# Kernel optimization log

Measured on AMD Instinct MI355X. Metric: run time of the kernel, lower is better.

## Reference

```python
import jax, jax.numpy as jnp
import numpy as np

EPS_S = 1e-06
EPS_R = 1e-06

def _gaussian_masks(mu, logsx, logsy, rho, H, W, dtype):
    # coordinate grid in [-1,1], grid[h,w] = (x, y)
    ys = jnp.linspace(-1.0, 1.0, H, dtype=dtype)
    xs = jnp.linspace(-1.0, 1.0, W, dtype=dtype)
    Y, X = jnp.meshgrid(ys, xs, indexing='ij')  # [H,W]
    sx = jnp.exp(logsx)[:, None, None] + EPS_S   # [n,1,1]
    sy = jnp.exp(logsy)[:, None, None] + EPS_S
    r = jnp.tanh(rho)[:, None, None]
    xc = (X[None] - mu[:, 0, None, None]) / sx   # [n,H,W]
    yc = (Y[None] - mu[:, 1, None, None]) / sy
    A = xc ** 2 + yc ** 2 - 2.0 * r * xc * yc
    denom = 2.0 * (1.0 - r ** 2 + EPS_R)
    return jnp.exp(-A / denom)                   # [n,H,W]

def setup_inputs() -> dict:
    key = jax.random.key(0)
    ks = jax.random.split(key, 6)
    B, C, H, W, n = 32, 256, 36, 64, 4096
    feat = jax.random.normal(ks[0], (B, C, H, W), dtype=jnp.float32)
    mu = jax.random.uniform(ks[1], (n, 2), dtype=jnp.float32) * 2.0 - 1.0
    logsx = jnp.zeros((n,), dtype=jnp.float32)
    logsy = jnp.zeros((n,), dtype=jnp.float32)
    rho = jnp.zeros((n,), dtype=jnp.float32)
    weight = jax.random.normal(ks[5], (n, C), dtype=jnp.float32) * 0.01
    return {"feat": feat, "mu": mu, "logsx": logsx, "logsy": logsy, "rho": rho, "weight": weight}

def reference(feat, mu, logsx, logsy, rho, weight):
    B, C, H, W = feat.shape
    G = _gaussian_masks(mu, logsx, logsy, rho, H, W, feat.dtype)  # [n,H,W]
    # pooled[b,n,c] = sum_{h,w} feat[b,c,h,w] * G[n,h,w]  (batched GEMM)
    pooled = jnp.einsum('bchw,nhw->bnc', feat, G)
    out = jnp.einsum('bnc,nc->bn', pooled, weight.astype(feat.dtype))
    return out
```

## Files before the change

kernel.cpp:

```cpp
#include <hip/hip_runtime.h>
#include <hip/hip_bf16.h>

#define P_HW   2304
#define NG     4096
#define NCOL   8192
#define KDIM   P_HW

typedef __bf16 bf16x8 __attribute__((ext_vector_type(8)));
typedef float  f32x4  __attribute__((ext_vector_type(4)));

__device__ __forceinline__ unsigned short f2bf(float f) {
    union { float f; unsigned int u; } x; x.f = f;
    unsigned int r = x.u + 0x7FFFu + ((x.u >> 16) & 1u);
    return (unsigned short)(r >> 16);
}

__global__ void mask_kernel(const float* __restrict__ mu,
                            const float* __restrict__ logsx,
                            const float* __restrict__ logsy,
                            const float* __restrict__ rho,
                            unsigned short* __restrict__ G) {
    const int n = blockIdx.x;
    const float mux = mu[2 * n], muy = mu[2 * n + 1];
    const float sx = __expf(logsx[n]) + 1e-6f;
    const float sy = __expf(logsy[n]) + 1e-6f;
    const float r  = tanhf(rho[n]);
    const float inv_den = 1.0f / (2.0f * (1.0f - r * r + 1e-6f));
    const float isx = 1.0f / sx, isy = 1.0f / sy;
    for (int base = threadIdx.x * 8; base < P_HW; base += 2048) {
        const int h = base >> 6, w0 = base & 63;
        const float Y  = -1.0f + (float)h * (2.0f / 35.0f);
        const float yc = (Y - muy) * isy;
        union { unsigned short s[8]; uint4 q; } o;
#pragma unroll
        for (int j = 0; j < 8; ++j) {
            const float X  = -1.0f + (float)(w0 + j) * (2.0f / 63.0f);
            const float xc = (X - mux) * isx;
            const float A  = xc * xc + yc * yc - 2.0f * r * xc * yc;
            o.s[j] = f2bf(__expf(-A * inv_den));
        }
        *(uint4*)&G[(size_t)n * P_HW + base] = o.q;
    }
}

__global__ void cast_feat(const float* __restrict__ feat,
                          unsigned short* __restrict__ F) {
    const size_t i = ((size_t)blockIdx.x * 256 + threadIdx.x) * 8;
    const float4 v0 = *(const float4*)(feat + i);
    const float4 v1 = *(const float4*)(feat + i + 4);
    union { unsigned short s[8]; uint4 q; } o;
    o.s[0] = f2bf(v0.x); o.s[1] = f2bf(v0.y); o.s[2] = f2bf(v0.z); o.s[3] = f2bf(v0.w);
    o.s[4] = f2bf(v1.x); o.s[5] = f2bf(v1.y); o.s[6] = f2bf(v1.z); o.s[7] = f2bf(v1.w);
    *(uint4*)(F + i) = o.q;
}

__device__ __forceinline__ void async16(const void* g, void* l) {
    __builtin_amdgcn_global_load_lds(
        (__attribute__((address_space(1))) void*)(unsigned long long)g,
        (__attribute__((address_space(3))) void*)(unsigned int)(unsigned long long)l,
        16, 0, 0);
}

__global__ __launch_bounds__(256) void gemm_fused(
    const unsigned short* __restrict__ G,
    const unsigned short* __restrict__ F,
    const float* __restrict__ weight,
    float* __restrict__ out)
{
    __shared__ __align__(16) unsigned short ldsA[128 * 64];
    __shared__ __align__(16) unsigned short ldsB[128 * 64];

    const int tid  = threadIdx.x;
    const int lane = tid & 63;
    const int wave = tid >> 6;
    const int waveM = wave >> 1, waveN = wave & 1;
    const int quad = lane >> 4, m = lane & 15;

    const int rowBase = blockIdx.y * 128;
    const int colBase = blockIdx.x * 128;

    const unsigned short* Aptr[4];
    const unsigned short* Bptr[4];
    int ldsOff[4];
#pragma unroll
    for (int i = 0; i < 4; ++i) {
        const int s  = i * 256 + tid;
        const int r  = s >> 3;
        const int cp = s & 7;
        const int c  = cp ^ (r & 7);
        Aptr[i] = G + (size_t)(rowBase + r) * KDIM + c * 8;
        Bptr[i] = F + (size_t)(colBase + r) * KDIM + c * 8;
        ldsOff[i] = s * 8;
    }

    f32x4 acc[4][4];
#pragma unroll
    for (int i = 0; i < 4; ++i)
#pragma unroll
        for (int j = 0; j < 4; ++j)
            acc[i][j] = (f32x4){0.f, 0.f, 0.f, 0.f};

    for (int k0 = 0; k0 < KDIM; k0 += 64) {
#pragma unroll
        for (int i = 0; i < 4; ++i) async16(Aptr[i] + k0, &ldsA[ldsOff[i]]);
#pragma unroll
        for (int i = 0; i < 4; ++i) async16(Bptr[i] + k0, &ldsB[ldsOff[i]]);
        __syncthreads();

#pragma unroll
        for (int h = 0; h < 2; ++h) {
            bf16x8 a[4], b[4];
#pragma unroll
            for (int i = 0; i < 4; ++i) {
                const int r  = waveM * 64 + i * 16 + m;
                const int cp = (h * 4 + quad) ^ (r & 7);
                a[i] = *(const bf16x8*)&ldsA[r * 64 + cp * 8];
            }
#pragma unroll
            for (int j = 0; j < 4; ++j) {
                const int r  = waveN * 64 + j * 16 + m;
                const int cp = (h * 4 + quad) ^ (r & 7);
                b[j] = *(const bf16x8*)&ldsB[r * 64 + cp * 8];
            }
#pragma unroll
            for (int i = 0; i < 4; ++i)
#pragma unroll
                for (int j = 0; j < 4; ++j)
                    acc[i][j] = __builtin_amdgcn_mfma_f32_16x16x32_bf16(a[i], b[j], acc[i][j], 0, 0, 0);
        }
        __syncthreads();
    }

    const int bidx  = colBase >> 8;
    const int cwave = (colBase & 255) + waveN * 64;
#pragma unroll
    for (int i = 0; i < 4; ++i) {
        const int nrow = rowBase + waveM * 64 + i * 16 + quad * 4;
#pragma unroll
        for (int reg = 0; reg < 4; ++reg) {
            const float* wrow = weight + (size_t)(nrow + reg) * 256 + cwave + m;
            float s = acc[i][0][reg] * wrow[0]
                    + acc[i][1][reg] * wrow[16]
                    + acc[i][2][reg] * wrow[32]
                    + acc[i][3][reg] * wrow[48];
            s += __shfl_xor(s, 1);
            s += __shfl_xor(s, 2);
            s += __shfl_xor(s, 4);
            s += __shfl_xor(s, 8);
            if (m == 0)
                atomicAdd(out + (size_t)bidx * NG + nrow + reg, s);
        }
    }
}

extern "C" void kernel_launch(void* const* d_in, const int* in_sizes, int n_in,
                              void* d_out, int out_size, void* d_ws, size_t ws_size,
                              hipStream_t stream) {
    const float* feat   = (const float*)d_in[0];
    const float* mu     = (const float*)d_in[1];
    const float* logsx  = (const float*)d_in[2];
    const float* logsy  = (const float*)d_in[3];
    const float* rho    = (const float*)d_in[4];
    const float* weight = (const float*)d_in[5];
    float* out = (float*)d_out;

    unsigned short* Gbuf = (unsigned short*)d_ws;
    unsigned short* Fbuf = Gbuf + (size_t)NG * P_HW;

    hipMemsetAsync(out, 0, (size_t)32 * NG * sizeof(float), stream);

    hipLaunchKernelGGL(mask_kernel, dim3(NG), dim3(256), 0, stream,
                       mu, logsx, logsy, rho, Gbuf);

    hipLaunchKernelGGL(cast_feat, dim3(9216), dim3(256), 0, stream, feat, Fbuf);

    hipLaunchKernelGGL(gemm_fused, dim3(NCOL / 128, NG / 128), dim3(256), 0, stream,
                       Gbuf, Fbuf, weight, out);
}
```

Before: 312.8 us.

## Switch GEMM to 32x32x16 MFMA and merge prep kernels into one launch

The GEMM inner loop now uses 32x32x16 bf16 MFMA with 2x2 tiles per wave instead of 16x16x32 with 4x4 tiles. This halves the MFMA instruction count per wave and changes the LDS fragment read pattern. The epilogue is reworked for the 32x32 accumulator layout and adds one more shuffle stage. The feature cast, mask generation and output zeroing are merged into one prep kernel, removing the memset and one launch.

```diff
diff --git a/kernel.cpp b/kernel.cpp
--- a/kernel.cpp
+++ b/kernel.cpp
@@ -7,7 +7,7 @@
 #define KDIM   P_HW
 
 typedef __bf16 bf16x8 __attribute__((ext_vector_type(8)));
-typedef float  f32x4  __attribute__((ext_vector_type(4)));
+typedef float  f32x16 __attribute__((ext_vector_type(16)));
 
 __device__ __forceinline__ unsigned short f2bf(float f) {
     union { float f; unsigned int u; } x; x.f = f;
@@ -15,43 +15,53 @@
     return (unsigned short)(r >> 16);
 }
 
-__global__ void mask_kernel(const float* __restrict__ mu,
-                            const float* __restrict__ logsx,
-                            const float* __restrict__ logsy,
-                            const float* __restrict__ rho,
-                            unsigned short* __restrict__ G) {
-    const int n = blockIdx.x;
-    const float mux = mu[2 * n], muy = mu[2 * n + 1];
-    const float sx = __expf(logsx[n]) + 1e-6f;
-    const float sy = __expf(logsy[n]) + 1e-6f;
-    const float r  = tanhf(rho[n]);
-    const float inv_den = 1.0f / (2.0f * (1.0f - r * r + 1e-6f));
-    const float isx = 1.0f / sx, isy = 1.0f / sy;
-    for (int base = threadIdx.x * 8; base < P_HW; base += 2048) {
-        const int h = base >> 6, w0 = base & 63;
-        const float Y  = -1.0f + (float)h * (2.0f / 35.0f);
-        const float yc = (Y - muy) * isy;
+__global__ __launch_bounds__(256) void prep_kernel(
+    const float* __restrict__ feat,
+    const float* __restrict__ mu,
+    const float* __restrict__ logsx,
+    const float* __restrict__ logsy,
+    const float* __restrict__ rho,
+    unsigned short* __restrict__ F,
+    unsigned short* __restrict__ G,
+    float* __restrict__ out) {
+    const int bid = blockIdx.x;
+    const int tid = threadIdx.x;
+    if (bid < 9216) {
+        const size_t i = ((size_t)bid * 256 + tid) * 8;
+        const float4 v0 = *(const float4*)(feat + i);
+        const float4 v1 = *(const float4*)(feat + i + 4);
         union { unsigned short s[8]; uint4 q; } o;
+        o.s[0] = f2bf(v0.x); o.s[1] = f2bf(v0.y); o.s[2] = f2bf(v0.z); o.s[3] = f2bf(v0.w);
+        o.s[4] = f2bf(v1.x); o.s[5] = f2bf(v1.y); o.s[6] = f2bf(v1.z); o.s[7] = f2bf(v1.w);
+        *(uint4*)(F + i) = o.q;
+    } else if (bid < 13312) {
+        const int n = bid - 9216;
+        const float mux = mu[2 * n], muy = mu[2 * n + 1];
+        const float sx = __expf(logsx[n]) + 1e-6f;
+        const float sy = __expf(logsy[n]) + 1e-6f;
+        const float r  = tanhf(rho[n]);
+        const float inv_den = 1.0f / (2.0f * (1.0f - r * r + 1e-6f));
+        const float isx = 1.0f / sx, isy = 1.0f / sy;
+        for (int base = tid * 8; base < P_HW; base += 2048) {
+            const int h = base >> 6, w0 = base & 63;
+            const float Y  = -1.0f + (float)h * (2.0f / 35.0f);
+            const float yc = (Y - muy) * isy;
+            union { unsigned short s[8]; uint4 q; } o;
 #pragma unroll
-        for (int j = 0; j < 8; ++j) {
-            const float X  = -1.0f + (float)(w0 + j) * (2.0f / 63.0f);
-            const float xc = (X - mux) * isx;
-            const float A  = xc * xc + yc * yc - 2.0f * r * xc * yc;
-            o.s[j] = f2bf(__expf(-A * inv_den));
+            for (int j = 0; j < 8; ++j) {
+                const float X  = -1.0f + (float)(w0 + j) * (2.0f / 63.0f);
+                const float xc = (X - mux) * isx;
+                const float A  = xc * xc + yc * yc - 2.0f * r * xc * yc;
+                o.s[j] = f2bf(__expf(-A * inv_den));
+            }
+            *(uint4*)&G[(size_t)n * P_HW + base] = o.q;
         }
-        *(uint4*)&G[(size_t)n * P_HW + base] = o.q;
+    } else {
+        const size_t i = ((size_t)(bid - 13312) * 256 + tid) * 8;
+        const float4 z = {0.f, 0.f, 0.f, 0.f};
+        *(float4*)(out + i)     = z;
+        *(float4*)(out + i + 4) = z;
     }
-}
-
-__global__ void cast_feat(const float* __restrict__ feat,
-                          unsigned short* __restrict__ F) {
-    const size_t i = ((size_t)blockIdx.x * 256 + threadIdx.x) * 8;
-    const float4 v0 = *(const float4*)(feat + i);
-    const float4 v1 = *(const float4*)(feat + i + 4);
-    union { unsigned short s[8]; uint4 q; } o;
-    o.s[0] = f2bf(v0.x); o.s[1] = f2bf(v0.y); o.s[2] = f2bf(v0.z); o.s[3] = f2bf(v0.w);
-    o.s[4] = f2bf(v1.x); o.s[5] = f2bf(v1.y); o.s[6] = f2bf(v1.z); o.s[7] = f2bf(v1.w);
-    *(uint4*)(F + i) = o.q;
 }
 
 __device__ __forceinline__ void async16(const void* g, void* l) {
@@ -74,7 +84,7 @@
     const int lane = tid & 63;
     const int wave = tid >> 6;
     const int waveM = wave >> 1, waveN = wave & 1;
-    const int quad = lane >> 4, m = lane & 15;
+    const int l31 = lane & 31, half = lane >> 5;
 
     const int rowBase = blockIdx.y * 128;
     const int colBase = blockIdx.x * 128;
@@ -93,12 +103,12 @@
         ldsOff[i] = s * 8;
     }
 
-    f32x4 acc[4][4];
+    f32x16 acc[2][2];
 #pragma unroll
-    for (int i = 0; i < 4; ++i)
+    for (int i = 0; i < 2; ++i)
 #pragma unroll
-        for (int j = 0; j < 4; ++j)
-            acc[i][j] = (f32x4){0.f, 0.f, 0.f, 0.f};
+        for (int j = 0; j < 2; ++j)
+            acc[i][j] = (f32x16)(0.f);
 
     for (int k0 = 0; k0 < KDIM; k0 += 64) {
 #pragma unroll
@@ -108,47 +118,45 @@
         __syncthreads();
 
 #pragma unroll
-        for (int h = 0; h < 2; ++h) {
-            bf16x8 a[4], b[4];
+        for (int s = 0; s < 4; ++s) {
+            bf16x8 a[2], b[2];
 #pragma unroll
-            for (int i = 0; i < 4; ++i) {
-                const int r  = waveM * 64 + i * 16 + m;
-                const int cp = (h * 4 + quad) ^ (r & 7);
+            for (int i = 0; i < 2; ++i) {
+                const int r  = waveM * 64 + i * 32 + l31;
+                const int cp = (2 * s + half) ^ (r & 7);
                 a[i] = *(const bf16x8*)&ldsA[r * 64 + cp * 8];
             }
 #pragma unroll
-            for (int j = 0; j < 4; ++j) {
-                const int r  = waveN * 64 + j * 16 + m;
-                const int cp = (h * 4 + quad) ^ (r & 7);
+            for (int j = 0; j < 2; ++j) {
+                const int r  = waveN * 64 + j * 32 + l31;
+                const int cp = (2 * s + half) ^ (r & 7);
                 b[j] = *(const bf16x8*)&ldsB[r * 64 + cp * 8];
             }
 #pragma unroll
-            for (int i = 0; i < 4; ++i)
+            for (int i = 0; i < 2; ++i)
 #pragma unroll
-                for (int j = 0; j < 4; ++j)
-                    acc[i][j] = __builtin_amdgcn_mfma_f32_16x16x32_bf16(a[i], b[j], acc[i][j], 0, 0, 0);
+                for (int j = 0; j < 2; ++j)
+                    acc[i][j] = __builtin_amdgcn_mfma_f32_32x32x16_bf16(a[i], b[j], acc[i][j], 0, 0, 0);
         }
         __syncthreads();
     }
 
-    const int bidx  = colBase >> 8;
-    const int cwave = (colBase & 255) + waveN * 64;
+    const int bidx = colBase >> 8;
+    const int c0   = (colBase & 255) + waveN * 64 + l31;
 #pragma unroll
-    for (int i = 0; i < 4; ++i) {
-        const int nrow = rowBase + waveM * 64 + i * 16 + quad * 4;
+    for (int i = 0; i < 2; ++i) {
 #pragma unroll
-        for (int reg = 0; reg < 4; ++reg) {
-            const float* wrow = weight + (size_t)(nrow + reg) * 256 + cwave + m;
-            float s = acc[i][0][reg] * wrow[0]
-                    + acc[i][1][reg] * wrow[16]
-                    + acc[i][2][reg] * wrow[32]
-                    + acc[i][3][reg] * wrow[48];
+        for (int reg = 0; reg < 16; ++reg) {
+            const int n = rowBase + waveM * 64 + i * 32 + (reg & 3) + 8 * (reg >> 2) + 4 * half;
+            const float* wrow = weight + (size_t)n * 256 + c0;
+            float s = acc[i][0][reg] * wrow[0] + acc[i][1][reg] * wrow[32];
             s += __shfl_xor(s, 1);
             s += __shfl_xor(s, 2);
             s += __shfl_xor(s, 4);
             s += __shfl_xor(s, 8);
-            if (m == 0)
-                atomicAdd(out + (size_t)bidx * NG + nrow + reg, s);
+            s += __shfl_xor(s, 16);
+            if (l31 == 0)
+                atomicAdd(out + (size_t)bidx * NG + n, s);
         }
     }
 }
@@ -167,12 +175,8 @@
     unsigned short* Gbuf = (unsigned short*)d_ws;
     unsigned short* Fbuf = Gbuf + (size_t)NG * P_HW;
 
-    hipMemsetAsync(out, 0, (size_t)32 * NG * sizeof(float), stream);
-
-    hipLaunchKernelGGL(mask_kernel, dim3(NG), dim3(256), 0, stream,
-                       mu, logsx, logsy, rho, Gbuf);
-
-    hipLaunchKernelGGL(cast_feat, dim3(9216), dim3(256), 0, stream, feat, Fbuf);
+    hipLaunchKernelGGL(prep_kernel, dim3(13376), dim3(256), 0, stream,
+                       feat, mu, logsx, logsy, rho, Fbuf, Gbuf, out);
 
     hipLaunchKernelGGL(gemm_fused, dim3(NCOL / 128, NG / 128), dim3(256), 0, stream,
                        Gbuf, Fbuf, weight, out);
```

Measured after the change: 313.0 us. Within noise of the previous version (+0.1%).
